# Performance work log

Hardware: AMD Instinct MI355X
Metric: run time of the kernel (lower is better)

The kernel has to match this reference:

```python
import jax, jax.numpy as jnp
import numpy as np

N_EMBD = 2048
N_HEAD = 16
D_HEAD = N_EMBD // N_HEAD  # 128
B, T = 2, 2048
ROPE_BASE = 10000.0


def _rope_cos_sin(T, d, dtype):
    # (T, d) cos/sin tables, rotate-half convention
    inv_freq = 1.0 / (ROPE_BASE ** (jnp.arange(0, d, 2, dtype=jnp.float32) / d))
    ang = jnp.arange(T, dtype=jnp.float32)[:, None] * inv_freq[None, :]  # (T, d/2)
    cos = jnp.concatenate([jnp.cos(ang), jnp.cos(ang)], axis=-1).astype(dtype)
    sin = jnp.concatenate([jnp.sin(ang), jnp.sin(ang)], axis=-1).astype(dtype)
    return cos, sin


def _rotate_half(x):
    d = x.shape[-1] // 2
    return jnp.concatenate([-x[..., d:], x[..., :d]], axis=-1)


def setup_inputs() -> dict:
    key = jax.random.key(0)
    k1, k2, k3 = jax.random.split(key, 3)
    x = jax.random.normal(k1, (B, T, N_EMBD), dtype=jnp.float32)
    w_qkv = jax.random.normal(k2, (3 * N_EMBD, N_EMBD), dtype=jnp.float32) * 0.02
    w_proj = jax.random.normal(k3, (N_EMBD, N_EMBD), dtype=jnp.float32) * 0.02
    return {"x": x, "w_qkv": w_qkv, "w_proj": w_proj}


def reference(x, w_qkv, w_proj):
    Bq, Tq, C = x.shape
    H, D = N_HEAD, D_HEAD
    # fused QKV projection (torch Linear: x @ W.T)
    qkv = jnp.einsum('btc,fc->btf', x, w_qkv).reshape(Bq, Tq, 3, H, D)
    q, k, v = qkv[:, :, 0], qkv[:, :, 1], qkv[:, :, 2]  # (B,T,H,D)
    q = jnp.transpose(q, (0, 2, 1, 3))  # (B,H,T,D)
    k = jnp.transpose(k, (0, 2, 1, 3))
    v = jnp.transpose(v, (0, 2, 1, 3))
    # RoPE (start_pos = 0)
    cos, sin = _rope_cos_sin(Tq, D, x.dtype)  # (T,D)
    q = q * cos[None, None] + _rotate_half(q) * sin[None, None]
    k = k * cos[None, None] + _rotate_half(k) * sin[None, None]
    # causal SDPA
    scale = 1.0 / jnp.sqrt(jnp.asarray(D, x.dtype))
    scores = jnp.einsum('bhqd,bhkd->bhqk', q, k) * scale  # (B,H,T,T)
    causal = jnp.tril(jnp.ones((Tq, Tq), dtype=bool))
    scores = jnp.where(causal[None, None], scores, jnp.asarray(-jnp.inf, x.dtype))
    attn = jax.nn.softmax(scores, axis=-1)
    y = jnp.einsum('bhqk,bhkd->bhqd', attn, v)  # (B,H,T,D)
    y = jnp.transpose(y, (0, 2, 1, 3)).reshape(Bq, Tq, C)
    y = jnp.einsum('btc,fc->btf', y, w_proj)
    return y
```

## Files before the change

kernel.cpp:

```cpp
#include <hip/hip_runtime.h>
#include <hip/hip_bf16.h>
#include <math.h>

typedef __attribute__((ext_vector_type(8))) short short8;
typedef __attribute__((ext_vector_type(4))) short short4_t;
typedef __attribute__((ext_vector_type(4))) float f32x4;

#define Bb 2
#define Tt 2048
#define Hh 16
#define Dd 128
#define Cc 2048
#define Ff 6144

__device__ __forceinline__ void gload_lds16(const void* g, void* l) {
  __builtin_amdgcn_global_load_lds(
      (const __attribute__((address_space(1))) void*)g,
      (__attribute__((address_space(3))) void*)l, 16, 0, 0);
}

__global__ __launch_bounds__(256) void cast_f32_bf16(
    const float* __restrict__ in, __hip_bfloat16* __restrict__ out, int n4)
{
  int i = blockIdx.x * 256 + threadIdx.x;
  if (i >= n4) return;
  float4 v = ((const float4*)in)[i];
  __hip_bfloat16 tmp[4] = {__float2bfloat16(v.x), __float2bfloat16(v.y),
                           __float2bfloat16(v.z), __float2bfloat16(v.w)};
  ((short4_t*)out)[i] = *(const short4_t*)tmp;
}

__device__ __forceinline__ void store_out(__hip_bfloat16* p, float v) { *p = __float2bfloat16(v); }
__device__ __forceinline__ void store_out(float* p, float v) { *p = v; }

template <typename OutT>
__global__ __launch_bounds__(256) void gemm_bt(
    const __hip_bfloat16* __restrict__ A,
    const __hip_bfloat16* __restrict__ Bm,
    OutT* __restrict__ Cm,
    int K, int N)
{
  __shared__ __align__(16) __hip_bfloat16 As[128 * 32];
  __shared__ __align__(16) __hip_bfloat16 Bs[128 * 32];
  const int tid  = threadIdx.x;
  const int wave = tid >> 6;
  const int lane = tid & 63;
  const int quad = lane >> 4;
  const int l16  = lane & 15;
  const int bm = blockIdx.y * 128;
  const int bn = blockIdx.x * 128;
  const int wm = (wave >> 1) * 64;
  const int wn = (wave & 1) * 64;

  f32x4 acc[4][4];
#pragma unroll
  for (int i = 0; i < 4; i++)
#pragma unroll
    for (int j = 0; j < 4; j++)
#pragma unroll
      for (int r = 0; r < 4; r++) acc[i][j][r] = 0.f;

  const int srow = lane >> 2;
  const int scol = (lane & 3) * 8;

  for (int k0 = 0; k0 < K; k0 += 32) {
#pragma unroll
    for (int c = 0; c < 2; c++) {
      int r0 = (wave * 2 + c) * 16;
      gload_lds16(A  + (size_t)(bm + r0 + srow) * K + k0 + scol, As + r0 * 32);
      gload_lds16(Bm + (size_t)(bn + r0 + srow) * K + k0 + scol, Bs + r0 * 32);
    }
    __syncthreads();
    short8 af[4], bf[4];
#pragma unroll
    for (int i = 0; i < 4; i++)
      af[i] = *(const short8*)(As + (wm + i * 16 + l16) * 32 + quad * 8);
#pragma unroll
    for (int j = 0; j < 4; j++)
      bf[j] = *(const short8*)(Bs + (wn + j * 16 + l16) * 32 + quad * 8);
#pragma unroll
    for (int i = 0; i < 4; i++)
#pragma unroll
      for (int j = 0; j < 4; j++)
        acc[i][j] = __builtin_amdgcn_mfma_f32_16x16x32_bf16(af[i], bf[j], acc[i][j], 0, 0, 0);
    __syncthreads();
  }

#pragma unroll
  for (int i = 0; i < 4; i++)
#pragma unroll
    for (int j = 0; j < 4; j++)
#pragma unroll
      for (int r = 0; r < 4; r++) {
        int gm = bm + wm + i * 16 + quad * 4 + r;
        int gn = bn + wn + j * 16 + l16;
        store_out(Cm + (size_t)gm * N + gn, acc[i][j][r]);
      }
}

__global__ __launch_bounds__(256) void rope_qk(__hip_bfloat16* __restrict__ qkv)
{
  int tid = blockIdx.x * 256 + threadIdx.x;
  int d = tid & 63;
  int h = (tid >> 6) & 15;
  int t = (tid >> 10) & 2047;
  int bw = tid >> 21;
  int b = bw & 1, which = bw >> 1;
  size_t base = (size_t)(b * Tt + t) * Ff + which * 2048 + h * Dd + d;
  float inv = expf(-(float)d * (9.210340371976184f / 64.0f));
  float ang = (float)t * inv;
  float c = cosf(ang), s = sinf(ang);
  float x1 = __bfloat162float(qkv[base]);
  float x2 = __bfloat162float(qkv[base + 64]);
  qkv[base]      = __float2bfloat16(x1 * c - x2 * s);
  qkv[base + 64] = __float2bfloat16(x2 * c + x1 * s);
}

__global__ __launch_bounds__(256) void transpose_v(
    const __hip_bfloat16* __restrict__ qkv, __hip_bfloat16* __restrict__ vt)
{
  __shared__ __hip_bfloat16 tile[64 * 65];
  int bh = blockIdx.y;
  int dt = blockIdx.x >> 5;
  int tt = blockIdx.x & 31;
  int b = bh >> 4, h = bh & 15;
  const __hip_bfloat16* src = qkv + (size_t)(b * Tt + tt * 64) * Ff + 4096 + h * Dd + dt * 64;
#pragma unroll
  for (int i = 0; i < 16; i++) {
    int lin = i * 256 + threadIdx.x;
    int tl = lin >> 6, dc = lin & 63;
    tile[tl * 65 + dc] = src[(size_t)tl * Ff + dc];
  }
  __syncthreads();
  __hip_bfloat16* dst = vt + ((size_t)bh * Dd + dt * 64) * Tt + tt * 64;
#pragma unroll
  for (int i = 0; i < 16; i++) {
    int lin = i * 256 + threadIdx.x;
    int dr = lin >> 6, tc = lin & 63;
    dst[(size_t)dr * Tt + tc] = tile[tc * 65 + dr];
  }
}

__global__ __launch_bounds__(256) void flash_attn2(
    const __hip_bfloat16* __restrict__ qkv,
    const __hip_bfloat16* __restrict__ vt,
    __hip_bfloat16* __restrict__ yat)
{
  __shared__ __align__(16) __hip_bfloat16 KsBuf[2][8192];
  __shared__ __align__(16) __hip_bfloat16 VsBuf[8192];
  __shared__ __align__(16) __hip_bfloat16 PsBuf[4 * 1088];
  const int tid  = threadIdx.x;
  const int wave = tid >> 6;
  const int lane = tid & 63;
  const int quad = lane >> 4;
  const int l16  = lane & 15;
  const int bh    = blockIdx.x & 31;
  const int pairp = blockIdx.x >> 5;
  const int b = bh >> 4, h = bh & 15;
  const float scale = 0.08838834764831845f;

  const char* kbase = (const char*)(qkv + (size_t)b * Tt * Ff + 2048 + h * Dd);
  const char* vbase = (const char*)(vt + (size_t)bh * Dd * Tt);
  __hip_bfloat16* Pw = PsBuf + wave * 1088;
  const int srow = lane & 15;
  const int scol = lane >> 4;

#pragma unroll 1
  for (int half = 0; half < 2; ++half) {
    const int qi = half ? (15 - pairp) : pairp;
    const int qm0 = qi * 128;
    const int niter = 2 * qi + 2;

    short8 qf[2][4];
#pragma unroll
    for (int mt = 0; mt < 2; mt++) {
      const __hip_bfloat16* qrow =
          qkv + (size_t)(b * Tt + qm0 + wave * 32 + mt * 16 + l16) * Ff + h * Dd;
#pragma unroll
      for (int kc = 0; kc < 4; kc++)
        qf[mt][kc] = *(const short8*)(qrow + kc * 32 + quad * 8);
    }

#pragma unroll
    for (int c = 0; c < 4; c++) {
      int chunk = wave * 4 + c;
      int j = chunk >> 2, kc = chunk & 3;
      const char* src = kbase + (size_t)(j * 16 + srow) * (Ff * 2) + kc * 64 + scol * 16;
      gload_lds16(src, KsBuf[0] + chunk * 512);
    }

    f32x4 oacc[2][8];
#pragma unroll
    for (int mt = 0; mt < 2; mt++)
#pragma unroll
      for (int jd = 0; jd < 8; jd++)
#pragma unroll
        for (int r = 0; r < 4; r++) oacc[mt][jd][r] = 0.f;
    float mrow[2][4], lrow[2][4];
#pragma unroll
    for (int mt = 0; mt < 2; mt++)
#pragma unroll
      for (int r = 0; r < 4; r++) { mrow[mt][r] = -INFINITY; lrow[mt][r] = 0.f; }

#pragma unroll 1
    for (int kt = 0; kt < niter; ++kt) {
      __builtin_amdgcn_s_barrier();
#pragma unroll
      for (int c = 0; c < 4; c++) {
        int chunk = wave * 4 + c;
        int jd = chunk >> 1, k2 = chunk & 1;
        const char* src = vbase + (size_t)(jd * 16 + srow) * (Tt * 2) + kt * 128 + k2 * 64 + scol * 16;
        gload_lds16(src, VsBuf + chunk * 512);
      }
      if (kt + 1 < niter) {
#pragma unroll
        for (int c = 0; c < 4; c++) {
          int chunk = wave * 4 + c;
          int j = chunk >> 2, kc = chunk & 3;
          const char* src = kbase + (size_t)((kt + 1) * 64 + j * 16 + srow) * (Ff * 2) + kc * 64 + scol * 16;
          gload_lds16(src, KsBuf[(kt + 1) & 1] + chunk * 512);
        }
        __builtin_amdgcn_s_waitcnt(0xF78);
      } else {
        __builtin_amdgcn_s_waitcnt(0xF74);
      }
      __builtin_amdgcn_s_barrier();

      const __hip_bfloat16* KsB = KsBuf[kt & 1];
      const bool diag = (kt >= 2 * qi);
      float pv1[4][4];

#pragma unroll
      for (int mt = 0; mt < 2; mt++) {
        f32x4 sacc[4];
#pragma unroll
        for (int j = 0; j < 4; j++)
#pragma unroll
          for (int r = 0; r < 4; r++) sacc[j][r] = 0.f;
#pragma unroll
        for (int j = 0; j < 4; j++)
#pragma unroll
          for (int kc = 0; kc < 4; kc++) {
            short8 kf = *(const short8*)(KsB + (j * 4 + kc) * 512 + lane * 8);
            sacc[j] = __builtin_amdgcn_mfma_f32_16x16x32_bf16(qf[mt][kc], kf, sacc[j], 0, 0, 0);
          }
        float sv[4][4];
#pragma unroll
        for (int j = 0; j < 4; j++)
#pragma unroll
          for (int r = 0; r < 4; r++) {
            float v = sacc[j][r] * scale;
            if (diag) {
              int kg = kt * 64 + j * 16 + l16;
              int qg = qm0 + wave * 32 + mt * 16 + quad * 4 + r;
              if (kg > qg) v = -INFINITY;
            }
            sv[j][r] = v;
          }
        float mnew[4];
#pragma unroll
        for (int r = 0; r < 4; r++) {
          float m = fmaxf(fmaxf(sv[0][r], sv[1][r]), fmaxf(sv[2][r], sv[3][r]));
          mnew[r] = m;
        }
#pragma unroll
        for (int off = 1; off < 16; off <<= 1)
#pragma unroll
          for (int r = 0; r < 4; r++)
            mnew[r] = fmaxf(mnew[r], __shfl_xor(mnew[r], off, 64));
        float alpha[4];
#pragma unroll
        for (int r = 0; r < 4; r++) {
          float mi = fmaxf(mrow[mt][r], mnew[r]);
          alpha[r] = __expf(mrow[mt][r] - mi);
          mrow[mt][r] = mi;
        }
        float rs[4] = {0.f, 0.f, 0.f, 0.f};
#pragma unroll
        for (int j = 0; j < 4; j++)
#pragma unroll
          for (int r = 0; r < 4; r++) {
            float p = __expf(sv[j][r] - mrow[mt][r]);
            rs[r] += p;
            if (mt == 0)
              Pw[(j * 2 + (l16 >> 3)) * 136 + (quad * 4 + r) * 8 + (l16 & 7)] = __float2bfloat16(p);
            else
              pv1[j][r] = p;
          }
#pragma unroll
        for (int off = 1; off < 16; off <<= 1)
#pragma unroll
          for (int r = 0; r < 4; r++)
            rs[r] += __shfl_xor(rs[r], off, 64);
#pragma unroll
        for (int r = 0; r < 4; r++) lrow[mt][r] = lrow[mt][r] * alpha[r] + rs[r];
#pragma unroll
        for (int jd = 0; jd < 8; jd++)
#pragma unroll
          for (int r = 0; r < 4; r++) oacc[mt][jd][r] *= alpha[r];
      }

      if (kt + 1 < niter) {
        __builtin_amdgcn_s_waitcnt(0xF74);
      } else {
        __builtin_amdgcn_s_waitcnt(0xF70);
      }
      __builtin_amdgcn_s_barrier();

#pragma unroll
      for (int k2 = 0; k2 < 2; k2++) {
        short8 pf = *(const short8*)(Pw + (k2 * 4 + quad) * 136 + l16 * 8);
#pragma unroll
        for (int jd = 0; jd < 8; jd++) {
          short8 vf = *(const short8*)(VsBuf + (jd * 2 + k2) * 512 + lane * 8);
          oacc[0][jd] = __builtin_amdgcn_mfma_f32_16x16x32_bf16(pf, vf, oacc[0][jd], 0, 0, 0);
        }
      }
#pragma unroll
      for (int j = 0; j < 4; j++)
#pragma unroll
        for (int r = 0; r < 4; r++)
          Pw[(j * 2 + (l16 >> 3)) * 136 + (quad * 4 + r) * 8 + (l16 & 7)] = __float2bfloat16(pv1[j][r]);
#pragma unroll
      for (int k2 = 0; k2 < 2; k2++) {
        short8 pf = *(const short8*)(Pw + (k2 * 4 + quad) * 136 + l16 * 8);
#pragma unroll
        for (int jd = 0; jd < 8; jd++) {
          short8 vf = *(const short8*)(VsBuf + (jd * 2 + k2) * 512 + lane * 8);
          oacc[1][jd] = __builtin_amdgcn_mfma_f32_16x16x32_bf16(pf, vf, oacc[1][jd], 0, 0, 0);
        }
      }
    }

#pragma unroll
    for (int mt = 0; mt < 2; mt++) {
      float linv[4];
#pragma unroll
      for (int r = 0; r < 4; r++) linv[r] = 1.f / lrow[mt][r];
#pragma unroll
      for (int jd = 0; jd < 8; jd++)
#pragma unroll
        for (int r = 0; r < 4; r++) {
          int trow = qm0 + wave * 32 + mt * 16 + quad * 4 + r;
          yat[(size_t)(b * Tt + trow) * Cc + h * Dd + jd * 16 + l16] =
              __float2bfloat16(oacc[mt][jd][r] * linv[r]);
        }
    }
  }
}

extern "C" void kernel_launch(void* const* d_in, const int* in_sizes, int n_in,
                              void* d_out, int out_size, void* d_ws, size_t ws_size,
                              hipStream_t stream) {
  (void)in_sizes; (void)n_in; (void)out_size; (void)ws_size;
  const float* x_f      = (const float*)d_in[0];
  const float* w_qkv_f  = (const float*)d_in[1];
  const float* w_proj_f = (const float*)d_in[2];
  float* out = (float*)d_out;

  char* ws = (char*)d_ws;
  __hip_bfloat16* qkv = (__hip_bfloat16*)ws;
  __hip_bfloat16* vt  = (__hip_bfloat16*)(ws + 50331648);
  __hip_bfloat16* yat = (__hip_bfloat16*)(ws + 67108864);
  __hip_bfloat16* xb  = (__hip_bfloat16*)(ws + 83886080);
  __hip_bfloat16* wqb = (__hip_bfloat16*)(ws + 100663296);
  __hip_bfloat16* wpb = (__hip_bfloat16*)(ws + 125829120);

  cast_f32_bf16<<<8192, 256, 0, stream>>>(x_f, xb, 2097152);
  cast_f32_bf16<<<12288, 256, 0, stream>>>(w_qkv_f, wqb, 3145728);
  cast_f32_bf16<<<4096, 256, 0, stream>>>(w_proj_f, wpb, 1048576);

  gemm_bt<__hip_bfloat16><<<dim3(48, 32), 256, 0, stream>>>(xb, wqb, qkv, 2048, 6144);
  rope_qk<<<32768, 256, 0, stream>>>(qkv);
  transpose_v<<<dim3(64, 32), 256, 0, stream>>>(qkv, vt);
  flash_attn2<<<256, 256, 0, stream>>>(qkv, vt, yat);
  gemm_bt<float><<<dim3(16, 32), 256, 0, stream>>>(yat, wpb, out, 2048, 2048);
}
```

Baseline: 478.3 us.

## Split attention query tile across 8 waves and fold softmax scale into RoPE

The flash attention kernel now uses 512 threads (8 waves), with each wave owning 16 query rows instead of 32. Per-wave register state (one oacc set, one row-stat set) halves, and each wave does half the K/V tile loads, which adds parallelism for the 256-block grid. The softmax scale is folded into the RoPE kernel's Q output, removing a multiply per score. Each K/V tile is now shared by more waves, at the cost of more barrier participants and some extra rounding from scaling Q before bf16 storage.

```diff
diff --git a/kernel.cpp b/kernel.cpp
--- a/kernel.cpp
+++ b/kernel.cpp
@@ -112,8 +112,14 @@
   float c = cosf(ang), s = sinf(ang);
   float x1 = __bfloat162float(qkv[base]);
   float x2 = __bfloat162float(qkv[base + 64]);
-  qkv[base]      = __float2bfloat16(x1 * c - x2 * s);
-  qkv[base + 64] = __float2bfloat16(x2 * c + x1 * s);
+  float o1 = x1 * c - x2 * s;
+  float o2 = x2 * c + x1 * s;
+  if (which == 0) {
+    o1 *= 0.08838834764831845f;
+    o2 *= 0.08838834764831845f;
+  }
+  qkv[base]      = __float2bfloat16(o1);
+  qkv[base + 64] = __float2bfloat16(o2);
 }
 
 __global__ __launch_bounds__(256) void transpose_v(
@@ -141,14 +147,14 @@
   }
 }
 
-__global__ __launch_bounds__(256) void flash_attn2(
+__global__ __launch_bounds__(512) void flash_attn3(
     const __hip_bfloat16* __restrict__ qkv,
     const __hip_bfloat16* __restrict__ vt,
     __hip_bfloat16* __restrict__ yat)
 {
   __shared__ __align__(16) __hip_bfloat16 KsBuf[2][8192];
   __shared__ __align__(16) __hip_bfloat16 VsBuf[8192];
-  __shared__ __align__(16) __hip_bfloat16 PsBuf[4 * 1088];
+  __shared__ __align__(16) __hip_bfloat16 PsBuf[8 * 1088];
   const int tid  = threadIdx.x;
   const int wave = tid >> 6;
   const int lane = tid & 63;
@@ -157,7 +163,6 @@
   const int bh    = blockIdx.x & 31;
   const int pairp = blockIdx.x >> 5;
   const int b = bh >> 4, h = bh & 15;
-  const float scale = 0.08838834764831845f;
 
   const char* kbase = (const char*)(qkv + (size_t)b * Tt * Ff + 2048 + h * Dd);
   const char* vbase = (const char*)(vt + (size_t)bh * Dd * Tt);
@@ -171,137 +176,123 @@
     const int qm0 = qi * 128;
     const int niter = 2 * qi + 2;
 
-    short8 qf[2][4];
-#pragma unroll
-    for (int mt = 0; mt < 2; mt++) {
+    short8 qf[4];
+    {
       const __hip_bfloat16* qrow =
-          qkv + (size_t)(b * Tt + qm0 + wave * 32 + mt * 16 + l16) * Ff + h * Dd;
+          qkv + (size_t)(b * Tt + qm0 + wave * 16 + l16) * Ff + h * Dd;
 #pragma unroll
       for (int kc = 0; kc < 4; kc++)
-        qf[mt][kc] = *(const short8*)(qrow + kc * 32 + quad * 8);
+        qf[kc] = *(const short8*)(qrow + kc * 32 + quad * 8);
     }
 
 #pragma unroll
-    for (int c = 0; c < 4; c++) {
-      int chunk = wave * 4 + c;
+    for (int c = 0; c < 2; c++) {
+      int chunk = wave * 2 + c;
       int j = chunk >> 2, kc = chunk & 3;
       const char* src = kbase + (size_t)(j * 16 + srow) * (Ff * 2) + kc * 64 + scol * 16;
       gload_lds16(src, KsBuf[0] + chunk * 512);
     }
 
-    f32x4 oacc[2][8];
-#pragma unroll
-    for (int mt = 0; mt < 2; mt++)
-#pragma unroll
-      for (int jd = 0; jd < 8; jd++)
-#pragma unroll
-        for (int r = 0; r < 4; r++) oacc[mt][jd][r] = 0.f;
-    float mrow[2][4], lrow[2][4];
-#pragma unroll
-    for (int mt = 0; mt < 2; mt++)
-#pragma unroll
-      for (int r = 0; r < 4; r++) { mrow[mt][r] = -INFINITY; lrow[mt][r] = 0.f; }
+    f32x4 oacc[8];
+#pragma unroll
+    for (int jd = 0; jd < 8; jd++)
+#pragma unroll
+      for (int r = 0; r < 4; r++) oacc[jd][r] = 0.f;
+    float mrow[4], lrow[4];
+#pragma unroll
+    for (int r = 0; r < 4; r++) { mrow[r] = -INFINITY; lrow[r] = 0.f; }
 
 #pragma unroll 1
     for (int kt = 0; kt < niter; ++kt) {
       __builtin_amdgcn_s_barrier();
 #pragma unroll
-      for (int c = 0; c < 4; c++) {
-        int chunk = wave * 4 + c;
+      for (int c = 0; c < 2; c++) {
+        int chunk = wave * 2 + c;
         int jd = chunk >> 1, k2 = chunk & 1;
         const char* src = vbase + (size_t)(jd * 16 + srow) * (Tt * 2) + kt * 128 + k2 * 64 + scol * 16;
         gload_lds16(src, VsBuf + chunk * 512);
       }
       if (kt + 1 < niter) {
 #pragma unroll
-        for (int c = 0; c < 4; c++) {
-          int chunk = wave * 4 + c;
+        for (int c = 0; c < 2; c++) {
+          int chunk = wave * 2 + c;
           int j = chunk >> 2, kc = chunk & 3;
           const char* src = kbase + (size_t)((kt + 1) * 64 + j * 16 + srow) * (Ff * 2) + kc * 64 + scol * 16;
           gload_lds16(src, KsBuf[(kt + 1) & 1] + chunk * 512);
         }
-        __builtin_amdgcn_s_waitcnt(0xF78);
+        __builtin_amdgcn_s_waitcnt(0xF74);
       } else {
-        __builtin_amdgcn_s_waitcnt(0xF74);
+        __builtin_amdgcn_s_waitcnt(0xF72);
       }
       __builtin_amdgcn_s_barrier();
 
       const __hip_bfloat16* KsB = KsBuf[kt & 1];
       const bool diag = (kt >= 2 * qi);
-      float pv1[4][4];
-
-#pragma unroll
-      for (int mt = 0; mt < 2; mt++) {
-        f32x4 sacc[4];
-#pragma unroll
-        for (int j = 0; j < 4; j++)
-#pragma unroll
-          for (int r = 0; r < 4; r++) sacc[j][r] = 0.f;
-#pragma unroll
-        for (int j = 0; j < 4; j++)
-#pragma unroll
-          for (int kc = 0; kc < 4; kc++) {
-            short8 kf = *(const short8*)(KsB + (j * 4 + kc) * 512 + lane * 8);
-            sacc[j] = __builtin_amdgcn_mfma_f32_16x16x32_bf16(qf[mt][kc], kf, sacc[j], 0, 0, 0);
+
+      f32x4 sacc[4];
+#pragma unroll
+      for (int j = 0; j < 4; j++)
+#pragma unroll
+        for (int r = 0; r < 4; r++) sacc[j][r] = 0.f;
+#pragma unroll
+      for (int j = 0; j < 4; j++)
+#pragma unroll
+        for (int kc = 0; kc < 4; kc++) {
+          short8 kf = *(const short8*)(KsB + (j * 4 + kc) * 512 + lane * 8);
+          sacc[j] = __builtin_amdgcn_mfma_f32_16x16x32_bf16(qf[kc], kf, sacc[j], 0, 0, 0);
+        }
+      float sv[4][4];
+#pragma unroll
+      for (int j = 0; j < 4; j++)
+#pragma unroll
+        for (int r = 0; r < 4; r++) {
+          float v = sacc[j][r];
+          if (diag) {
+            int kg = kt * 64 + j * 16 + l16;
+            int qg = qm0 + wave * 16 + quad * 4 + r;
+            if (kg > qg) v = -INFINITY;
           }
-        float sv[4][4];
-#pragma unroll
-        for (int j = 0; j < 4; j++)
-#pragma unroll
-          for (int r = 0; r < 4; r++) {
-            float v = sacc[j][r] * scale;
-            if (diag) {
-              int kg = kt * 64 + j * 16 + l16;
-              int qg = qm0 + wave * 32 + mt * 16 + quad * 4 + r;
-              if (kg > qg) v = -INFINITY;
-            }
-            sv[j][r] = v;
-          }
-        float mnew[4];
+          sv[j][r] = v;
+        }
+      float mnew[4];
+#pragma unroll
+      for (int r = 0; r < 4; r++)
+        mnew[r] = fmaxf(fmaxf(sv[0][r], sv[1][r]), fmaxf(sv[2][r], sv[3][r]));
+#pragma unroll
+      for (int off = 1; off < 16; off <<= 1)
+#pragma unroll
+        for (int r = 0; r < 4; r++)
+          mnew[r] = fmaxf(mnew[r], __shfl_xor(mnew[r], off, 64));
+      float alpha[4];
+#pragma unroll
+      for (int r = 0; r < 4; r++) {
+        float mi = fmaxf(mrow[r], mnew[r]);
+        alpha[r] = __expf(mrow[r] - mi);
+        mrow[r] = mi;
+      }
+      float rs[4] = {0.f, 0.f, 0.f, 0.f};
+#pragma unroll
+      for (int j = 0; j < 4; j++)
 #pragma unroll
         for (int r = 0; r < 4; r++) {
-          float m = fmaxf(fmaxf(sv[0][r], sv[1][r]), fmaxf(sv[2][r], sv[3][r]));
-          mnew[r] = m;
-        }
-#pragma unroll
-        for (int off = 1; off < 16; off <<= 1)
-#pragma unroll
-          for (int r = 0; r < 4; r++)
-            mnew[r] = fmaxf(mnew[r], __shfl_xor(mnew[r], off, 64));
-        float alpha[4];
-#pragma unroll
-        for (int r = 0; r < 4; r++) {
-          float mi = fmaxf(mrow[mt][r], mnew[r]);
-          alpha[r] = __expf(mrow[mt][r] - mi);
-          mrow[mt][r] = mi;
-        }
-        float rs[4] = {0.f, 0.f, 0.f, 0.f};
-#pragma unroll
-        for (int j = 0; j < 4; j++)
-#pragma unroll
-          for (int r = 0; r < 4; r++) {
-            float p = __expf(sv[j][r] - mrow[mt][r]);
-            rs[r] += p;
-            if (mt == 0)
-              Pw[(j * 2 + (l16 >> 3)) * 136 + (quad * 4 + r) * 8 + (l16 & 7)] = __float2bfloat16(p);
-            else
-              pv1[j][r] = p;
-          }
-#pragma unroll
-        for (int off = 1; off < 16; off <<= 1)
-#pragma unroll
-          for (int r = 0; r < 4; r++)
-            rs[r] += __shfl_xor(rs[r], off, 64);
-#pragma unroll
-        for (int r = 0; r < 4; r++) lrow[mt][r] = lrow[mt][r] * alpha[r] + rs[r];
-#pragma unroll
-        for (int jd = 0; jd < 8; jd++)
-#pragma unroll
-          for (int r = 0; r < 4; r++) oacc[mt][jd][r] *= alpha[r];
-      }
+          float p = __expf(sv[j][r] - mrow[r]);
+          rs[r] += p;
+          Pw[(j * 2 + (l16 >> 3)) * 136 + (quad * 4 + r) * 8 + (l16 & 7)] = __float2bfloat16(p);
+        }
+#pragma unroll
+      for (int off = 1; off < 16; off <<= 1)
+#pragma unroll
+        for (int r = 0; r < 4; r++)
+          rs[r] += __shfl_xor(rs[r], off, 64);
+#pragma unroll
+      for (int r = 0; r < 4; r++) lrow[r] = lrow[r] * alpha[r] + rs[r];
+#pragma unroll
+      for (int jd = 0; jd < 8; jd++)
+#pragma unroll
+        for (int r = 0; r < 4; r++) oacc[jd][r] *= alpha[r];
 
       if (kt + 1 < niter) {
-        __builtin_amdgcn_s_waitcnt(0xF74);
+        __builtin_amdgcn_s_waitcnt(0xF72);
       } else {
         __builtin_amdgcn_s_waitcnt(0xF70);
       }
@@ -313,39 +304,22 @@
 #pragma unroll
         for (int jd = 0; jd < 8; jd++) {
           short8 vf = *(const short8*)(VsBuf + (jd * 2 + k2) * 512 + lane * 8);
-          oacc[0][jd] = __builtin_amdgcn_mfma_f32_16x16x32_bf16(pf, vf, oacc[0][jd], 0, 0, 0);
-        }
-      }
-#pragma unroll
-      for (int j = 0; j < 4; j++)
-#pragma unroll
-        for (int r = 0; r < 4; r++)
-          Pw[(j * 2 + (l16 >> 3)) * 136 + (quad * 4 + r) * 8 + (l16 & 7)] = __float2bfloat16(pv1[j][r]);
-#pragma unroll
-      for (int k2 = 0; k2 < 2; k2++) {
-        short8 pf = *(const short8*)(Pw + (k2 * 4 + quad) * 136 + l16 * 8);
-#pragma unroll
-        for (int jd = 0; jd < 8; jd++) {
-          short8 vf = *(const short8*)(VsBuf + (jd * 2 + k2) * 512 + lane * 8);
-          oacc[1][jd] = __builtin_amdgcn_mfma_f32_16x16x32_bf16(pf, vf, oacc[1][jd], 0, 0, 0);
+          oacc[jd] = __builtin_amdgcn_mfma_f32_16x16x32_bf16(pf, vf, oacc[jd], 0, 0, 0);
         }
       }
     }
 
-#pragma unroll
-    for (int mt = 0; mt < 2; mt++) {
-      float linv[4];
-#pragma unroll
-      for (int r = 0; r < 4; r++) linv[r] = 1.f / lrow[mt][r];
-#pragma unroll
-      for (int jd = 0; jd < 8; jd++)
-#pragma unroll
-        for (int r = 0; r < 4; r++) {
-          int trow = qm0 + wave * 32 + mt * 16 + quad * 4 + r;
-          yat[(size_t)(b * Tt + trow) * Cc + h * Dd + jd * 16 + l16] =
-              __float2bfloat16(oacc[mt][jd][r] * linv[r]);
-        }
-    }
+    float linv[4];
+#pragma unroll
+    for (int r = 0; r < 4; r++) linv[r] = 1.f / lrow[r];
+#pragma unroll
+    for (int jd = 0; jd < 8; jd++)
+#pragma unroll
+      for (int r = 0; r < 4; r++) {
+        int trow = qm0 + wave * 16 + quad * 4 + r;
+        yat[(size_t)(b * Tt + trow) * Cc + h * Dd + jd * 16 + l16] =
+            __float2bfloat16(oacc[jd][r] * linv[r]);
+      }
   }
 }
 
@@ -373,6 +347,6 @@
   gemm_bt<__hip_bfloat16><<<dim3(48, 32), 256, 0, stream>>>(xb, wqb, qkv, 2048, 6144);
   rope_qk<<<32768, 256, 0, stream>>>(qkv);
   transpose_v<<<dim3(64, 32), 256, 0, stream>>>(qkv, vt);
-  flash_attn2<<<256, 256, 0, stream>>>(qkv, vt, yat);
+  flash_attn3<<<256, 512, 0, stream>>>(qkv, vt, yat);
   gemm_bt<float><<<dim3(16, 32), 256, 0, stream>>>(yat, wpb, out, 2048, 2048);
 }
```

After: 462.5 us. -3.3%, faster.
